# Performance work log

Hardware: AMD Instinct MI355X
Metric: run time of the kernel (lower is better)

Reference implementation:

```python
import jax, jax.numpy as jnp
import numpy as np

B, S, D, H = 2, 2048, 1024, 16
DH = D // H


def setup_inputs() -> dict:
    key = jax.random.key(0)
    ks = jax.random.split(key, 12)
    sc = 1.0 / np.sqrt(D)
    return {
        "query": jax.random.normal(ks[0], (B, S, D), jnp.float32),
        "key": jax.random.normal(ks[1], (B, S, D), jnp.float32),
        "value": jax.random.normal(ks[2], (B, S, D), jnp.float32),
        "key_mask": jax.random.randint(ks[3], (B, S), 0, 2, jnp.int32),
        "Wq": jax.random.normal(ks[4], (D, D), jnp.float32) * sc,
        "bq": jnp.zeros((D,), jnp.float32),
        "Wk": jax.random.normal(ks[5], (D, D), jnp.float32) * sc,
        "bk": jnp.zeros((D,), jnp.float32),
        "Wv": jax.random.normal(ks[6], (D, D), jnp.float32) * sc,
        "bv": jnp.zeros((D,), jnp.float32),
        "Wo": jax.random.normal(ks[7], (D, D), jnp.float32) * sc,
        "bo": jnp.zeros((D,), jnp.float32),
    }


def _shape(x):
    # (B, L, D) -> (B, H, L, DH)
    return x.reshape(B, -1, H, DH).transpose(0, 2, 1, 3)


def reference(query, key, value, key_mask, Wq, bq, Wk, bk, Wv, bv, Wo, bo):
    # linear projections (torch Linear: x @ W.T + b)
    q = _shape(query @ Wq.T + bq)  # (B,H,S,DH)
    k = _shape(key @ Wk.T + bk)
    v = _shape(value @ Wv.T + bv)

    q = q / jnp.sqrt(jnp.asarray(DH, q.dtype))
    scores = jnp.einsum("bhqd,bhkd->bhqk", q, k)  # (B,H,S,S)

    pad = (key_mask == 0)[:, None, None, :]  # (B,1,1,K)
    scores = jnp.where(pad, jnp.asarray(-1e18, scores.dtype), scores)
    attn = jax.nn.softmax(scores, axis=-1)
    attn = jnp.where(pad, jnp.asarray(0.0, attn.dtype), attn)
    # dropout p=0.0 (eval) -> identity

    ctx = jnp.einsum("bhqk,bhkd->bhqd", attn, v)
    ctx = ctx.transpose(0, 2, 1, 3).reshape(B, -1, D)  # unshape
    output = ctx @ Wo.T + bo
    return (output, attn)
```

## Files before the change

### kernel.cpp

```cpp
#include <hip/hip_runtime.h>

#define B_  2
#define S_  2048
#define D_  1024
#define H_  16
#define DH_ 64

typedef _Float16 f16;
typedef f16   f16x2 __attribute__((ext_vector_type(2)));
typedef f16   f16x4 __attribute__((ext_vector_type(4)));
typedef f16   f16x8 __attribute__((ext_vector_type(8)));
typedef float f32x4 __attribute__((ext_vector_type(4)));
typedef float f32x16 __attribute__((ext_vector_type(16)));

static __device__ __forceinline__ f16x8 ldsm8(const f16* p) {
    return *reinterpret_cast<const f16x8*>(p);
}

static __device__ __forceinline__ int swz(int row, int byteInRow) {
    return row * 128 + (byteInRow ^ ((row & 7) << 4));
}

static __device__ __forceinline__ void gll16(const void* g, void* l) {
    __builtin_amdgcn_global_load_lds(
        (const __attribute__((address_space(1))) void*)g,
        (__attribute__((address_space(3))) void*)l, 16, 0, 0);
}

static __device__ __forceinline__ unsigned pk16(float a, float b) {
    return __builtin_bit_cast(unsigned, __builtin_amdgcn_cvt_pkrtz(a, b));
}

__global__ __launch_bounds__(256)
void qkv_gemm(const float* __restrict__ Aq, const float* __restrict__ Ak,
              const float* __restrict__ Av,
              const float* __restrict__ Wq, const float* __restrict__ Wk,
              const float* __restrict__ Wv,
              const float* __restrict__ bq, const float* __restrict__ bk,
              const float* __restrict__ bv,
              f16* __restrict__ qo, f16* __restrict__ ko, f16* __restrict__ vo,
              float qscale)
{
    constexpr int K = 1024, N = 1024;
    __shared__ __align__(16) f16 As[128][40];
    __shared__ __align__(16) f16 Bs[128][40];
    const int z = blockIdx.z;
    const float* A    = z == 0 ? Aq : z == 1 ? Ak : Av;
    const float* W    = z == 0 ? Wq : z == 1 ? Wk : Wv;
    const float* bias = z == 0 ? bq : z == 1 ? bk : bv;
    const float scale = z == 0 ? qscale : 1.0f;

    const int t  = threadIdx.x;
    const int bm = blockIdx.y * 128;
    const int bn = blockIdx.x * 128;
    const int w  = t >> 6, l = t & 63;
    const int wr = w >> 1, wc = w & 1;
    const int lr = l & 15, lg = l >> 4;

    f32x4 acc[4][4];
    #pragma unroll
    for (int m = 0; m < 4; ++m)
        #pragma unroll
        for (int n = 0; n < 4; ++n)
            acc[m][n] = (f32x4){0.f, 0.f, 0.f, 0.f};

    for (int kt = 0; kt < K / 32; ++kt) {
        #pragma unroll
        for (int i = 0; i < 4; ++i) {
            int idx = t + i * 256;
            int row = idx >> 3, g = idx & 7;
            float4 v = *reinterpret_cast<const float4*>(A + (size_t)(bm + row) * K + kt * 32 + g * 4);
            alignas(8) f16 hh[4] = {(f16)v.x, (f16)v.y, (f16)v.z, (f16)v.w};
            *reinterpret_cast<uint2*>(&As[row][g * 4]) = *reinterpret_cast<uint2*>(hh);
        }
        #pragma unroll
        for (int i = 0; i < 4; ++i) {
            int idx = t + i * 256;
            int row = idx >> 3, g = idx & 7;
            float4 v = *reinterpret_cast<const float4*>(W + (size_t)(bn + row) * K + kt * 32 + g * 4);
            alignas(8) f16 hh[4] = {(f16)v.x, (f16)v.y, (f16)v.z, (f16)v.w};
            *reinterpret_cast<uint2*>(&Bs[row][g * 4]) = *reinterpret_cast<uint2*>(hh);
        }
        __syncthreads();

        f16x8 af[4], bfv[4];
        #pragma unroll
        for (int m = 0; m < 4; ++m) af[m]  = ldsm8(&As[wr * 64 + m * 16 + lr][lg * 8]);
        #pragma unroll
        for (int n = 0; n < 4; ++n) bfv[n] = ldsm8(&Bs[wc * 64 + n * 16 + lr][lg * 8]);
        #pragma unroll
        for (int m = 0; m < 4; ++m)
            #pragma unroll
            for (int n = 0; n < 4; ++n)
                acc[m][n] = __builtin_amdgcn_mfma_f32_16x16x32_f16(af[m], bfv[n], acc[m][n], 0, 0, 0);
        __syncthreads();
    }

    #pragma unroll
    for (int m = 0; m < 4; ++m) {
        #pragma unroll
        for (int n = 0; n < 4; ++n) {
            int col = bn + wc * 64 + n * 16 + lr;
            float bb = bias[col];
            if (z == 2) {
                int row0 = bm + wr * 64 + m * 16 + lg * 4;
                int b = row0 >> 11, s = row0 & 2047;
                int hh_ = col >> 6, d = col & 63;
                alignas(8) f16 hv[4];
                #pragma unroll
                for (int j = 0; j < 4; ++j)
                    hv[j] = (f16)(acc[m][n][j] + bb);
                *reinterpret_cast<uint2*>(vo +
                    (((size_t)(b * 16 + hh_) * 64 + d) * 2048 + s)) =
                    *reinterpret_cast<uint2*>(hv);
            } else {
                f16* Cp = z == 0 ? qo : ko;
                #pragma unroll
                for (int j = 0; j < 4; ++j) {
                    int row = bm + wr * 64 + m * 16 + lg * 4 + j;
                    Cp[(size_t)row * N + col] = (f16)((acc[m][n][j] + bb) * scale);
                }
            }
        }
    }
}

__global__ __launch_bounds__(256)
void gemm_out(const f16* __restrict__ A, const float* __restrict__ W,
              const float* __restrict__ bias, float* __restrict__ Cp)
{
    constexpr int K = 1024, N = 1024;
    __shared__ __align__(16) f16 As[128][40];
    __shared__ __align__(16) f16 Bs[128][40];
    const int t  = threadIdx.x;
    const int bm = blockIdx.y * 128;
    const int bn = blockIdx.x * 128;
    const int w  = t >> 6, l = t & 63;
    const int wr = w >> 1, wc = w & 1;
    const int lr = l & 15, lg = l >> 4;

    f32x4 acc[4][4];
    #pragma unroll
    for (int m = 0; m < 4; ++m)
        #pragma unroll
        for (int n = 0; n < 4; ++n)
            acc[m][n] = (f32x4){0.f, 0.f, 0.f, 0.f};

    for (int kt = 0; kt < K / 32; ++kt) {
        #pragma unroll
        for (int i = 0; i < 2; ++i) {
            int idx = t + i * 256;
            int row = idx >> 2, g = idx & 3;
            *reinterpret_cast<uint4*>(&As[row][g * 8]) =
                *reinterpret_cast<const uint4*>(A + (size_t)(bm + row) * K + kt * 32 + g * 8);
        }
        #pragma unroll
        for (int i = 0; i < 4; ++i) {
            int idx = t + i * 256;
            int row = idx >> 3, g = idx & 7;
            float4 v = *reinterpret_cast<const float4*>(W + (size_t)(bn + row) * K + kt * 32 + g * 4);
            alignas(8) f16 hh[4] = {(f16)v.x, (f16)v.y, (f16)v.z, (f16)v.w};
            *reinterpret_cast<uint2*>(&Bs[row][g * 4]) = *reinterpret_cast<uint2*>(hh);
        }
        __syncthreads();

        f16x8 af[4], bfv[4];
        #pragma unroll
        for (int m = 0; m < 4; ++m) af[m]  = ldsm8(&As[wr * 64 + m * 16 + lr][lg * 8]);
        #pragma unroll
        for (int n = 0; n < 4; ++n) bfv[n] = ldsm8(&Bs[wc * 64 + n * 16 + lr][lg * 8]);
        #pragma unroll
        for (int m = 0; m < 4; ++m)
            #pragma unroll
            for (int n = 0; n < 4; ++n)
                acc[m][n] = __builtin_amdgcn_mfma_f32_16x16x32_f16(af[m], bfv[n], acc[m][n], 0, 0, 0);
        __syncthreads();
    }

    #pragma unroll
    for (int m = 0; m < 4; ++m) {
        #pragma unroll
        for (int n = 0; n < 4; ++n) {
            int col = bn + wc * 64 + n * 16 + lr;
            float bb = bias[col];
            #pragma unroll
            for (int j = 0; j < 4; ++j) {
                int row = bm + wr * 64 + m * 16 + lg * 4 + j;
                Cp[(size_t)row * N + col] = acc[m][n][j] + bb;
            }
        }
    }
}

__global__ __launch_bounds__(512, 4)
void k_sums(const f16* __restrict__ qh, const f16* __restrict__ khp,
            const int* __restrict__ kmask, float* __restrict__ linv_g)
{
    __shared__ __align__(16) f16 ksd[2][64 * 64];
    __shared__ float red[4][32];
    __shared__ unsigned mbits[64];

    const int t  = threadIdx.x;
    const int w  = t >> 6, l = t & 63, lo = l & 31, hi = l >> 5;
    const int wq = w >> 1, wk = w & 1;

    const int bid  = blockIdx.x;
    const int xcd  = bid & 7;
    const int slot = bid >> 3;
    const int bh   = (xcd << 2) | (slot >> 4);
    const int qt   = slot & 15;
    const int b    = bh >> 4;
    const int h    = bh & 15;
    const int q0   = qt * 128;

    f16x8 qf[4];
    {
        const f16* qb = qh + (size_t)(b * S_ + q0 + wq * 32 + lo) * D_ + h * DH_ + hi * 8;
        #pragma unroll
        for (int c = 0; c < 4; ++c) qf[c] = *reinterpret_cast<const f16x8*>(qb + c * 16);
    }

    #pragma unroll
    for (int r = 0; r < 4; ++r) {
        int ktm = w * 4 + r;
        int mkv = kmask[b * S_ + ktm * 64 + l];
        unsigned long long bl = __ballot(mkv != 0);
        if (l == 0) {
            mbits[ktm * 2]     = (unsigned)bl;
            mbits[ktm * 2 + 1] = (unsigned)(bl >> 32);
        }
    }

    const int r8 = l >> 3, l8 = l & 7;
    const int xorc8 = (l8 ^ r8) * 8;
    const f16* kgb = khp + (size_t)b * S_ * D_ + h * DH_;
    const int krow = wk * 32 + lo;

    auto stageK = [&](int buf, int kt) {
        int row = w * 8 + r8;
        gll16(kgb + (size_t)(kt * 64 + row) * D_ + xorc8,
              (char*)ksd[buf] + w * 1024);
    };

    stageK(0, 0);
    __syncthreads();

    float ls = 0.f;
    int cur = 0;
    for (int kt = 0; kt < 32; ++kt) {
        if (kt + 1 < 32) stageK(cur ^ 1, kt + 1);

        const unsigned mshift = mbits[kt * 2 + wk] >> (hi * 4);

        f32x16 s;
        #pragma unroll
        for (int i = 0; i < 16; ++i) s[i] = 0.f;
        #pragma unroll
        for (int c = 0; c < 4; ++c) {
            f16x8 kf = *reinterpret_cast<const f16x8*>(
                (const char*)ksd[cur] + swz(krow, c * 32 + hi * 16));
            s = __builtin_amdgcn_mfma_f32_32x32x16_f16(kf, qf[c], s, 0, 0, 0);
        }
        #pragma unroll
        for (int q4 = 0; q4 < 4; ++q4)
            #pragma unroll
            for (int j = 0; j < 4; ++j) {
                float e = __builtin_amdgcn_exp2f(s[q4 * 4 + j]);
                ls += ((mshift >> (q4 * 8 + j)) & 1) ? e : 0.0f;
            }
        __syncthreads();
        cur ^= 1;
    }

    ls += __shfl_xor(ls, 32, 64);
    if (wk == 1 && hi == 0) red[wq][lo] = ls;
    __syncthreads();
    if (wk == 0 && hi == 0)
        linv_g[(size_t)bh * S_ + q0 + wq * 32 + lo] = 1.0f / (ls + red[wq][lo]);
}

__global__ __launch_bounds__(256, 3)
void attn_fused(const f16* __restrict__ qh, const f16* __restrict__ khp,
                const f16* __restrict__ vtg, const int* __restrict__ kmask,
                const float* __restrict__ linv_g,
                float* __restrict__ attn_out, f16* __restrict__ ch)
{
    __shared__ __align__(16) f16 ksd[2][64 * 64];
    __shared__ __align__(16) f16 vsd[2][64 * 64];
    __shared__ unsigned mbits[64];

    const int t   = threadIdx.x;
    const int w   = t >> 6, l = t & 63, lo = l & 31, hi = l >> 5;
    const int qh_ = w & 1, kh_ = w >> 1;

    const int bid  = blockIdx.x;
    const int xcd  = bid & 7;
    const int slot = bid >> 3;
    const int bh   = (xcd << 2) | (slot >> 5);
    const int qt   = slot & 31;
    const int b    = bh >> 4;
    const int h    = bh & 15;
    const int q0   = qt * 64;

    const float invl = linv_g[(size_t)bh * S_ + q0 + qh_ * 32 + lo];

    f16x8 qf[4];
    {
        const f16* qb = qh + (size_t)(b * S_ + q0 + qh_ * 32 + lo) * D_ + h * DH_ + hi * 8;
        #pragma unroll
        for (int c = 0; c < 4; ++c) qf[c] = *reinterpret_cast<const f16x8*>(qb + c * 16);
    }

    #pragma unroll
    for (int r = 0; r < 8; ++r) {
        int ktm = w * 8 + r;
        int mkv = kmask[b * S_ + ktm * 64 + l];
        unsigned long long bl = __ballot(mkv != 0);
        if (l == 0) {
            mbits[ktm * 2]     = (unsigned)bl;
            mbits[ktm * 2 + 1] = (unsigned)(bl >> 32);
        }
    }

    const int r8 = l >> 3, l8 = l & 7;
    const int xorc8 = (l8 ^ r8) * 8;
    const f16* kgb = khp + (size_t)b * S_ * D_ + h * DH_;
    const f16* vgb = vtg + (size_t)(bh * 64) * S_;
    const int krow = kh_ * 32 + lo;

    auto stageK = [&](int buf, int kt) {
        #pragma unroll
        for (int i = 0; i < 2; ++i) {
            int row = i * 32 + w * 8 + r8;
            gll16(kgb + (size_t)(kt * 64 + row) * D_ + xorc8,
                  (char*)ksd[buf] + i * 4096 + w * 1024);
        }
    };
    auto stageV = [&](int buf, int kt) {
        #pragma unroll
        for (int i = 0; i < 2; ++i) {
            int row = i * 32 + w * 8 + r8;
            gll16(vgb + (size_t)row * S_ + kt * 64 + xorc8,
                  (char*)vsd[buf] + i * 4096 + w * 1024);
        }
    };

    stageK(0, 0);
    stageV(0, 0);
    __syncthreads();

    f32x16 oc0, oc1;
    #pragma unroll
    for (int i = 0; i < 16; ++i) { oc0[i] = 0.f; oc1[i] = 0.f; }
    int cur = 0;

    float* ab = attn_out + ((size_t)((b * H_ + h) * S_ + q0 + qh_ * 32 + lo)) * S_
                + kh_ * 32 + hi * 4;

    for (int kt = 0; kt < 32; ++kt) {
        if (kt + 1 < 32) { stageK(cur ^ 1, kt + 1); stageV(cur ^ 1, kt + 1); }

        const unsigned mshift = mbits[kt * 2 + kh_] >> (hi * 4);

        f32x16 s;
        #pragma unroll
        for (int i = 0; i < 16; ++i) s[i] = 0.f;
        #pragma unroll
        for (int c = 0; c < 4; ++c) {
            f16x8 kf = *reinterpret_cast<const f16x8*>(
                (const char*)ksd[cur] + swz(krow, c * 32 + hi * 16));
            s = __builtin_amdgcn_mfma_f32_32x32x16_f16(kf, qf[c], s, 0, 0, 0);
        }

        float p[16];
        #pragma unroll
        for (int q4 = 0; q4 < 4; ++q4)
            #pragma unroll
            for (int j = 0; j < 4; ++j) {
                float e = __builtin_amdgcn_exp2f(s[q4 * 4 + j]);
                p[q4 * 4 + j] = ((mshift >> (q4 * 8 + j)) & 1) ? e : 0.0f;
            }

        #pragma unroll
        for (int q4 = 0; q4 < 4; ++q4) {
            float4 o = {p[q4 * 4 + 0] * invl, p[q4 * 4 + 1] * invl,
                        p[q4 * 4 + 2] * invl, p[q4 * 4 + 3] * invl};
            *reinterpret_cast<float4*>(ab + (size_t)kt * 64 + q4 * 8) = o;
        }

        #pragma unroll
        for (int j2 = 0; j2 < 2; ++j2) {
            unsigned wds[4], ods[4];
            #pragma unroll
            for (int i = 0; i < 4; ++i)
                wds[i] = pk16(p[8 * j2 + 2 * i], p[8 * j2 + 2 * i + 1]);
            #pragma unroll
            for (int i = 0; i < 4; ++i)
                ods[i] = (unsigned)__shfl_xor((int)wds[i], 32, 64);
            uint4 bw = (hi == 0) ? (uint4){wds[0], wds[1], ods[0], ods[1]}
                                 : (uint4){ods[2], ods[3], wds[2], wds[3]};
            f16x8 bf = __builtin_bit_cast(f16x8, bw);

            int bir = kh_ * 64 + j2 * 32 + hi * 16;
            f16x8 va0 = *reinterpret_cast<const f16x8*>((const char*)vsd[cur] + swz(lo, bir));
            f16x8 va1 = *reinterpret_cast<const f16x8*>((const char*)vsd[cur] + swz(lo + 32, bir));
            oc0 = __builtin_amdgcn_mfma_f32_32x32x16_f16(va0, bf, oc0, 0, 0, 0);
            oc1 = __builtin_amdgcn_mfma_f32_32x32x16_f16(va1, bf, oc1, 0, 0, 0);
        }
        __syncthreads();
        cur ^= 1;
    }

    float* psf = reinterpret_cast<float*>(&ksd[0][0]);
    #pragma unroll
    for (int g = 0; g < 2; ++g) {
        if (kh_ == 1 && qh_ == g) {
            #pragma unroll
            for (int r = 0; r < 16; ++r) {
                int d0 = (r & 3) + 8 * (r >> 2) + 4 * hi;
                psf[d0 * 32 + lo]        = oc0[r];
                psf[(32 + d0) * 32 + lo] = oc1[r];
            }
        }
        __syncthreads();
        if (kh_ == 0 && qh_ == g) {
            f16* cb = ch + (size_t)(b * S_ + q0 + g * 32 + lo) * D_ + h * DH_;
            #pragma unroll
            for (int q4 = 0; q4 < 4; ++q4) {
                int d0 = 8 * q4 + 4 * hi;
                f16x4 v0, v1;
                #pragma unroll
                for (int j = 0; j < 4; ++j) {
                    int r = 4 * q4 + j;
                    int dd = (r & 3) + 8 * (r >> 2) + 4 * hi;
                    v0[j] = (f16)((oc0[r] + psf[dd * 32 + lo]) * invl);
                    v1[j] = (f16)((oc1[r] + psf[(32 + dd) * 32 + lo]) * invl);
                }
                *reinterpret_cast<f16x4*>(cb + d0) = v0;
                *reinterpret_cast<f16x4*>(cb + 32 + d0) = v1;
            }
        }
        __syncthreads();
    }
}

extern "C" void kernel_launch(void* const* d_in, const int* in_sizes, int n_in,
                              void* d_out, int out_size, void* d_ws, size_t ws_size,
                              hipStream_t stream) {
    const float* query = (const float*)d_in[0];
    const float* key   = (const float*)d_in[1];
    const float* value = (const float*)d_in[2];
    const int*   kmask = (const int*)d_in[3];
    const float* Wq = (const float*)d_in[4];
    const float* bq = (const float*)d_in[5];
    const float* Wk = (const float*)d_in[6];
    const float* bk = (const float*)d_in[7];
    const float* Wv = (const float*)d_in[8];
    const float* bv = (const float*)d_in[9];
    const float* Wo = (const float*)d_in[10];
    const float* bo = (const float*)d_in[11];

    float* out  = (float*)d_out;
    float* attn = out + (size_t)B_ * S_ * D_;

    const size_t NE = (size_t)B_ * S_ * D_;
    f16* qhp = (f16*)d_ws;
    f16* khp = qhp + NE;
    f16* vtg = khp + NE;
    f16* chx = vtg + NE;
    float* linv_g = (float*)(chx + NE);

    const float qscale = 0.125f * 1.44269504088896340736f;

    qkv_gemm<<<dim3(8, 32, 3), 256, 0, stream>>>(query, key, value, Wq, Wk, Wv,
                                                 bq, bk, bv, qhp, khp, vtg, qscale);

    k_sums<<<dim3(B_ * H_ * (S_ / 128)), dim3(512), 0, stream>>>(qhp, khp, kmask, linv_g);

    attn_fused<<<dim3(B_ * H_ * (S_ / 64)), 256, 0, stream>>>(qhp, khp, vtg, kmask,
                                                              linv_g, attn, chx);

    gemm_out<<<dim3(8, 32), 256, 0, stream>>>(chx, Wo, bo, out);
}
```

Before: 337.1 us.

## Triple-buffer K/V staging with counted waits and nontemporal attention stores

The fused attention kernel moves from double to triple buffering of the K and V tiles in LDS. It now prefetches two tiles ahead and replaces the full __syncthreads with s_waitcnt vmcnt plus a raw barrier, so loads stay in flight across iterations. The large fp32 attention-probability writes now use nontemporal stores to reduce cache pollution. This costs extra LDS, which may reduce occupancy. The correctness of the hand-counted vmcnt values depends on how the global stores are counted.

```diff
diff --git a/kernel.cpp b/kernel.cpp
--- a/kernel.cpp
+++ b/kernel.cpp
@@ -285,8 +285,8 @@
                 const float* __restrict__ linv_g,
                 float* __restrict__ attn_out, f16* __restrict__ ch)
 {
-    __shared__ __align__(16) f16 ksd[2][64 * 64];
-    __shared__ __align__(16) f16 vsd[2][64 * 64];
+    __shared__ __align__(16) f16 ksd[3][64 * 64];
+    __shared__ __align__(16) f16 vsd[3][64 * 64];
     __shared__ unsigned mbits[64];
 
     const int t   = threadIdx.x;
@@ -328,26 +328,21 @@
     const f16* vgb = vtg + (size_t)(bh * 64) * S_;
     const int krow = kh_ * 32 + lo;
 
-    auto stageK = [&](int buf, int kt) {
+    auto stageKV = [&](int buf, int kt) {
         #pragma unroll
         for (int i = 0; i < 2; ++i) {
             int row = i * 32 + w * 8 + r8;
             gll16(kgb + (size_t)(kt * 64 + row) * D_ + xorc8,
-                  (char*)ksd[buf] + i * 4096 + w * 1024);
+                  (char*)ksd + buf * 8192 + i * 4096 + w * 1024);
+            gll16(vgb + (size_t)row * S_ + kt * 64 + xorc8,
+                  (char*)vsd + buf * 8192 + i * 4096 + w * 1024);
         }
     };
-    auto stageV = [&](int buf, int kt) {
-        #pragma unroll
-        for (int i = 0; i < 2; ++i) {
-            int row = i * 32 + w * 8 + r8;
-            gll16(vgb + (size_t)row * S_ + kt * 64 + xorc8,
-                  (char*)vsd[buf] + i * 4096 + w * 1024);
-        }
-    };
-
-    stageK(0, 0);
-    stageV(0, 0);
-    __syncthreads();
+
+    stageKV(0, 0);
+    stageKV(1, 1);
+    asm volatile("s_waitcnt vmcnt(4) lgkmcnt(0)" ::: "memory");
+    __builtin_amdgcn_s_barrier();
 
     f32x16 oc0, oc1;
     #pragma unroll
@@ -358,7 +353,10 @@
                 + kh_ * 32 + hi * 4;
 
     for (int kt = 0; kt < 32; ++kt) {
-        if (kt + 1 < 32) { stageK(cur ^ 1, kt + 1); stageV(cur ^ 1, kt + 1); }
+        if (kt + 2 < 32) {
+            int stg = cur + 2; if (stg >= 3) stg -= 3;
+            stageKV(stg, kt + 2);
+        }
 
         const unsigned mshift = mbits[kt * 2 + kh_] >> (hi * 4);
 
@@ -368,7 +366,7 @@
         #pragma unroll
         for (int c = 0; c < 4; ++c) {
             f16x8 kf = *reinterpret_cast<const f16x8*>(
-                (const char*)ksd[cur] + swz(krow, c * 32 + hi * 16));
+                (const char*)ksd + cur * 8192 + swz(krow, c * 32 + hi * 16));
             s = __builtin_amdgcn_mfma_f32_32x32x16_f16(kf, qf[c], s, 0, 0, 0);
         }
 
@@ -383,9 +381,10 @@
 
         #pragma unroll
         for (int q4 = 0; q4 < 4; ++q4) {
-            float4 o = {p[q4 * 4 + 0] * invl, p[q4 * 4 + 1] * invl,
-                        p[q4 * 4 + 2] * invl, p[q4 * 4 + 3] * invl};
-            *reinterpret_cast<float4*>(ab + (size_t)kt * 64 + q4 * 8) = o;
+            f32x4 o = {p[q4 * 4 + 0] * invl, p[q4 * 4 + 1] * invl,
+                       p[q4 * 4 + 2] * invl, p[q4 * 4 + 3] * invl};
+            __builtin_nontemporal_store(o,
+                reinterpret_cast<f32x4*>(ab + (size_t)kt * 64 + q4 * 8));
         }
 
         #pragma unroll
@@ -402,16 +401,21 @@
             f16x8 bf = __builtin_bit_cast(f16x8, bw);
 
             int bir = kh_ * 64 + j2 * 32 + hi * 16;
-            f16x8 va0 = *reinterpret_cast<const f16x8*>((const char*)vsd[cur] + swz(lo, bir));
-            f16x8 va1 = *reinterpret_cast<const f16x8*>((const char*)vsd[cur] + swz(lo + 32, bir));
+            f16x8 va0 = *reinterpret_cast<const f16x8*>(
+                (const char*)vsd + cur * 8192 + swz(lo, bir));
+            f16x8 va1 = *reinterpret_cast<const f16x8*>(
+                (const char*)vsd + cur * 8192 + swz(lo + 32, bir));
             oc0 = __builtin_amdgcn_mfma_f32_32x32x16_f16(va0, bf, oc0, 0, 0, 0);
             oc1 = __builtin_amdgcn_mfma_f32_32x32x16_f16(va1, bf, oc1, 0, 0, 0);
         }
-        __syncthreads();
-        cur ^= 1;
+
+        asm volatile("s_waitcnt vmcnt(8)" ::: "memory");
+        __builtin_amdgcn_s_barrier();
+        ++cur; if (cur >= 3) cur -= 3;
     }
 
     float* psf = reinterpret_cast<float*>(&ksd[0][0]);
+    __syncthreads();
     #pragma unroll
     for (int g = 0; g < 2; ++g) {
         if (kh_ == 1 && qh_ == g) {
```

Measured after the change: 753.7 us. +123.6%, slower.

## Fuse softmax row-sum pass into attention kernel with full-key-tile warps

Applied to the files above, without the earlier changes.

Removes the separate k_sums kernel and computes the softmax denominator inside attn_fused with a first pass over K, then a second pass that writes attention probabilities and accumulates P·V. Each warp now owns 32 query rows across all 64 keys of a tile, so the cross-warp LDS reduction of partial outputs at the end disappears. The grid shrinks to 128-query blocks (512 blocks of 256 threads) with 4 warps each doing 32 rows. This drops one launch and the linv round trip through global memory, but each block does more serial work, there are fewer blocks in flight, and register pressure rises.

```diff
diff --git a/kernel.cpp b/kernel.cpp
--- a/kernel.cpp
+++ b/kernel.cpp
@@ -192,17 +192,18 @@
     }
 }
 
-__global__ __launch_bounds__(512, 4)
-void k_sums(const f16* __restrict__ qh, const f16* __restrict__ khp,
-            const int* __restrict__ kmask, float* __restrict__ linv_g)
+__global__ __launch_bounds__(256, 3)
+void attn_fused(const f16* __restrict__ qh, const f16* __restrict__ khp,
+                const f16* __restrict__ vtg, const int* __restrict__ kmask,
+                float* __restrict__ attn_out, f16* __restrict__ ch)
 {
     __shared__ __align__(16) f16 ksd[2][64 * 64];
-    __shared__ float red[4][32];
+    __shared__ __align__(16) f16 vsd[2][64 * 64];
     __shared__ unsigned mbits[64];
 
     const int t  = threadIdx.x;
     const int w  = t >> 6, l = t & 63, lo = l & 31, hi = l >> 5;
-    const int wq = w >> 1, wk = w & 1;
+    const bool H1 = (hi == 1);
 
     const int bid  = blockIdx.x;
     const int xcd  = bid & 7;
@@ -212,101 +213,11 @@
     const int b    = bh >> 4;
     const int h    = bh & 15;
     const int q0   = qt * 128;
+    const int row  = q0 + w * 32 + lo;
 
     f16x8 qf[4];
     {
-        const f16* qb = qh + (size_t)(b * S_ + q0 + wq * 32 + lo) * D_ + h * DH_ + hi * 8;
-        #pragma unroll
-        for (int c = 0; c < 4; ++c) qf[c] = *reinterpret_cast<const f16x8*>(qb + c * 16);
-    }
-
-    #pragma unroll
-    for (int r = 0; r < 4; ++r) {
-        int ktm = w * 4 + r;
-        int mkv = kmask[b * S_ + ktm * 64 + l];
-        unsigned long long bl = __ballot(mkv != 0);
-        if (l == 0) {
-            mbits[ktm * 2]     = (unsigned)bl;
-            mbits[ktm * 2 + 1] = (unsigned)(bl >> 32);
-        }
-    }
-
-    const int r8 = l >> 3, l8 = l & 7;
-    const int xorc8 = (l8 ^ r8) * 8;
-    const f16* kgb = khp + (size_t)b * S_ * D_ + h * DH_;
-    const int krow = wk * 32 + lo;
-
-    auto stageK = [&](int buf, int kt) {
-        int row = w * 8 + r8;
-        gll16(kgb + (size_t)(kt * 64 + row) * D_ + xorc8,
-              (char*)ksd[buf] + w * 1024);
-    };
-
-    stageK(0, 0);
-    __syncthreads();
-
-    float ls = 0.f;
-    int cur = 0;
-    for (int kt = 0; kt < 32; ++kt) {
-        if (kt + 1 < 32) stageK(cur ^ 1, kt + 1);
-
-        const unsigned mshift = mbits[kt * 2 + wk] >> (hi * 4);
-
-        f32x16 s;
-        #pragma unroll
-        for (int i = 0; i < 16; ++i) s[i] = 0.f;
-        #pragma unroll
-        for (int c = 0; c < 4; ++c) {
-            f16x8 kf = *reinterpret_cast<const f16x8*>(
-                (const char*)ksd[cur] + swz(krow, c * 32 + hi * 16));
-            s = __builtin_amdgcn_mfma_f32_32x32x16_f16(kf, qf[c], s, 0, 0, 0);
-        }
-        #pragma unroll
-        for (int q4 = 0; q4 < 4; ++q4)
-            #pragma unroll
-            for (int j = 0; j < 4; ++j) {
-                float e = __builtin_amdgcn_exp2f(s[q4 * 4 + j]);
-                ls += ((mshift >> (q4 * 8 + j)) & 1) ? e : 0.0f;
-            }
-        __syncthreads();
-        cur ^= 1;
-    }
-
-    ls += __shfl_xor(ls, 32, 64);
-    if (wk == 1 && hi == 0) red[wq][lo] = ls;
-    __syncthreads();
-    if (wk == 0 && hi == 0)
-        linv_g[(size_t)bh * S_ + q0 + wq * 32 + lo] = 1.0f / (ls + red[wq][lo]);
-}
-
-__global__ __launch_bounds__(256, 3)
-void attn_fused(const f16* __restrict__ qh, const f16* __restrict__ khp,
-                const f16* __restrict__ vtg, const int* __restrict__ kmask,
-                const float* __restrict__ linv_g,
-                float* __restrict__ attn_out, f16* __restrict__ ch)
-{
-    __shared__ __align__(16) f16 ksd[2][64 * 64];
-    __shared__ __align__(16) f16 vsd[2][64 * 64];
-    __shared__ unsigned mbits[64];
-
-    const int t   = threadIdx.x;
-    const int w   = t >> 6, l = t & 63, lo = l & 31, hi = l >> 5;
-    const int qh_ = w & 1, kh_ = w >> 1;
-
-    const int bid  = blockIdx.x;
-    const int xcd  = bid & 7;
-    const int slot = bid >> 3;
-    const int bh   = (xcd << 2) | (slot >> 5);
-    const int qt   = slot & 31;
-    const int b    = bh >> 4;
-    const int h    = bh & 15;
-    const int q0   = qt * 64;
-
-    const float invl = linv_g[(size_t)bh * S_ + q0 + qh_ * 32 + lo];
-
-    f16x8 qf[4];
-    {
-        const f16* qb = qh + (size_t)(b * S_ + q0 + qh_ * 32 + lo) * D_ + h * DH_ + hi * 8;
+        const f16* qb = qh + (size_t)(b * S_ + row) * D_ + h * DH_ + hi * 8;
         #pragma unroll
         for (int c = 0; c < 4; ++c) qf[c] = *reinterpret_cast<const f16x8*>(qb + c * 16);
     }
@@ -326,24 +237,65 @@
     const int xorc8 = (l8 ^ r8) * 8;
     const f16* kgb = khp + (size_t)b * S_ * D_ + h * DH_;
     const f16* vgb = vtg + (size_t)(bh * 64) * S_;
-    const int krow = kh_ * 32 + lo;
 
     auto stageK = [&](int buf, int kt) {
         #pragma unroll
         for (int i = 0; i < 2; ++i) {
-            int row = i * 32 + w * 8 + r8;
-            gll16(kgb + (size_t)(kt * 64 + row) * D_ + xorc8,
-                  (char*)ksd[buf] + i * 4096 + w * 1024);
+            int rr = i * 32 + w * 8 + r8;
+            gll16(kgb + (size_t)(kt * 64 + rr) * D_ + xorc8,
+                  (char*)ksd + buf * 8192 + i * 4096 + w * 1024);
         }
     };
     auto stageV = [&](int buf, int kt) {
         #pragma unroll
         for (int i = 0; i < 2; ++i) {
-            int row = i * 32 + w * 8 + r8;
-            gll16(vgb + (size_t)row * S_ + kt * 64 + xorc8,
-                  (char*)vsd[buf] + i * 4096 + w * 1024);
+            int rr = i * 32 + w * 8 + r8;
+            gll16(vgb + (size_t)rr * S_ + kt * 64 + xorc8,
+                  (char*)vsd + buf * 8192 + i * 4096 + w * 1024);
         }
     };
+
+    stageK(0, 0);
+    __syncthreads();
+
+    float ls = 0.f;
+    int cur = 0;
+    for (int kt = 0; kt < 32; ++kt) {
+        if (kt + 1 < 32) stageK(cur ^ 1, kt + 1);
+
+        f32x16 s0, s1;
+        #pragma unroll
+        for (int i = 0; i < 16; ++i) { s0[i] = 0.f; s1[i] = 0.f; }
+        #pragma unroll
+        for (int c = 0; c < 4; ++c) {
+            f16x8 kf = *reinterpret_cast<const f16x8*>(
+                (const char*)ksd + cur * 8192 + swz(lo, c * 32 + hi * 16));
+            s0 = __builtin_amdgcn_mfma_f32_32x32x16_f16(kf, qf[c], s0, 0, 0, 0);
+        }
+        #pragma unroll
+        for (int c = 0; c < 4; ++c) {
+            f16x8 kf = *reinterpret_cast<const f16x8*>(
+                (const char*)ksd + cur * 8192 + swz(lo + 32, c * 32 + hi * 16));
+            s1 = __builtin_amdgcn_mfma_f32_32x32x16_f16(kf, qf[c], s1, 0, 0, 0);
+        }
+
+        const unsigned m0 = mbits[kt * 2]     >> (hi * 4);
+        const unsigned m1 = mbits[kt * 2 + 1] >> (hi * 4);
+        #pragma unroll
+        for (int q4 = 0; q4 < 4; ++q4)
+            #pragma unroll
+            for (int j = 0; j < 4; ++j) {
+                float e0 = __builtin_amdgcn_exp2f(s0[q4 * 4 + j]);
+                float e1 = __builtin_amdgcn_exp2f(s1[q4 * 4 + j]);
+                ls += ((m0 >> (q4 * 8 + j)) & 1) ? e0 : 0.0f;
+                ls += ((m1 >> (q4 * 8 + j)) & 1) ? e1 : 0.0f;
+            }
+        __syncthreads();
+        cur ^= 1;
+    }
+
+    ls += __shfl_xor(ls, 32, 64);
+    const float invl = 1.0f / ls;
 
     stageK(0, 0);
     stageV(0, 0);
@@ -352,95 +304,96 @@
     f32x16 oc0, oc1;
     #pragma unroll
     for (int i = 0; i < 16; ++i) { oc0[i] = 0.f; oc1[i] = 0.f; }
-    int cur = 0;
-
-    float* ab = attn_out + ((size_t)((b * H_ + h) * S_ + q0 + qh_ * 32 + lo)) * S_
-                + kh_ * 32 + hi * 4;
+    cur = 0;
+
+    float* ab = attn_out + ((size_t)bh * S_ + row) * S_ + hi * 4;
 
     for (int kt = 0; kt < 32; ++kt) {
         if (kt + 1 < 32) { stageK(cur ^ 1, kt + 1); stageV(cur ^ 1, kt + 1); }
 
-        const unsigned mshift = mbits[kt * 2 + kh_] >> (hi * 4);
-
-        f32x16 s;
-        #pragma unroll
-        for (int i = 0; i < 16; ++i) s[i] = 0.f;
+        f32x16 s0, s1;
+        #pragma unroll
+        for (int i = 0; i < 16; ++i) { s0[i] = 0.f; s1[i] = 0.f; }
         #pragma unroll
         for (int c = 0; c < 4; ++c) {
             f16x8 kf = *reinterpret_cast<const f16x8*>(
-                (const char*)ksd[cur] + swz(krow, c * 32 + hi * 16));
-            s = __builtin_amdgcn_mfma_f32_32x32x16_f16(kf, qf[c], s, 0, 0, 0);
-        }
-
-        float p[16];
+                (const char*)ksd + cur * 8192 + swz(lo, c * 32 + hi * 16));
+            s0 = __builtin_amdgcn_mfma_f32_32x32x16_f16(kf, qf[c], s0, 0, 0, 0);
+        }
+        #pragma unroll
+        for (int c = 0; c < 4; ++c) {
+            f16x8 kf = *reinterpret_cast<const f16x8*>(
+                (const char*)ksd + cur * 8192 + swz(lo + 32, c * 32 + hi * 16));
+            s1 = __builtin_amdgcn_mfma_f32_32x32x16_f16(kf, qf[c], s1, 0, 0, 0);
+        }
+
+        const unsigned m0 = mbits[kt * 2]     >> (hi * 4);
+        const unsigned m1 = mbits[kt * 2 + 1] >> (hi * 4);
+        float p0[16], p1[16];
         #pragma unroll
         for (int q4 = 0; q4 < 4; ++q4)
             #pragma unroll
             for (int j = 0; j < 4; ++j) {
-                float e = __builtin_amdgcn_exp2f(s[q4 * 4 + j]);
-                p[q4 * 4 + j] = ((mshift >> (q4 * 8 + j)) & 1) ? e : 0.0f;
+                float e0 = __builtin_amdgcn_exp2f(s0[q4 * 4 + j]);
+                float e1 = __builtin_amdgcn_exp2f(s1[q4 * 4 + j]);
+                p0[q4 * 4 + j] = ((m0 >> (q4 * 8 + j)) & 1) ? e0 : 0.0f;
+                p1[q4 * 4 + j] = ((m1 >> (q4 * 8 + j)) & 1) ? e1 : 0.0f;
             }
 
         #pragma unroll
         for (int q4 = 0; q4 < 4; ++q4) {
-            float4 o = {p[q4 * 4 + 0] * invl, p[q4 * 4 + 1] * invl,
-                        p[q4 * 4 + 2] * invl, p[q4 * 4 + 3] * invl};
-            *reinterpret_cast<float4*>(ab + (size_t)kt * 64 + q4 * 8) = o;
-        }
-
-        #pragma unroll
-        for (int j2 = 0; j2 < 2; ++j2) {
-            unsigned wds[4], ods[4];
-            #pragma unroll
-            for (int i = 0; i < 4; ++i)
-                wds[i] = pk16(p[8 * j2 + 2 * i], p[8 * j2 + 2 * i + 1]);
-            #pragma unroll
-            for (int i = 0; i < 4; ++i)
-                ods[i] = (unsigned)__shfl_xor((int)wds[i], 32, 64);
-            uint4 bw = (hi == 0) ? (uint4){wds[0], wds[1], ods[0], ods[1]}
-                                 : (uint4){ods[2], ods[3], wds[2], wds[3]};
-            f16x8 bf = __builtin_bit_cast(f16x8, bw);
-
-            int bir = kh_ * 64 + j2 * 32 + hi * 16;
-            f16x8 va0 = *reinterpret_cast<const f16x8*>((const char*)vsd[cur] + swz(lo, bir));
-            f16x8 va1 = *reinterpret_cast<const f16x8*>((const char*)vsd[cur] + swz(lo + 32, bir));
-            oc0 = __builtin_amdgcn_mfma_f32_32x32x16_f16(va0, bf, oc0, 0, 0, 0);
-            oc1 = __builtin_amdgcn_mfma_f32_32x32x16_f16(va1, bf, oc1, 0, 0, 0);
+            f32x4 o0 = {p0[q4 * 4 + 0] * invl, p0[q4 * 4 + 1] * invl,
+                        p0[q4 * 4 + 2] * invl, p0[q4 * 4 + 3] * invl};
+            *reinterpret_cast<f32x4*>(ab + (size_t)kt * 64 + q4 * 8) = o0;
+            f32x4 o1 = {p1[q4 * 4 + 0] * invl, p1[q4 * 4 + 1] * invl,
+                        p1[q4 * 4 + 2] * invl, p1[q4 * 4 + 3] * invl};
+            *reinterpret_cast<f32x4*>(ab + (size_t)kt * 64 + 32 + q4 * 8) = o1;
+        }
+
+        unsigned wa[2][4], wb[2][4];
+        #pragma unroll
+        for (int q4 = 0; q4 < 4; ++q4) {
+            wa[0][q4] = pk16(p0[q4 * 4 + 0], p0[q4 * 4 + 1]);
+            wb[0][q4] = pk16(p0[q4 * 4 + 2], p0[q4 * 4 + 3]);
+            wa[1][q4] = pk16(p1[q4 * 4 + 0], p1[q4 * 4 + 1]);
+            wb[1][q4] = pk16(p1[q4 * 4 + 2], p1[q4 * 4 + 3]);
+        }
+
+        #pragma unroll
+        for (int c2 = 0; c2 < 4; ++c2) {
+            const int hh = c2 >> 1, base = (c2 & 1) * 2;
+            unsigned a0 = wa[hh][base], a1 = wa[hh][base + 1];
+            unsigned b0 = wb[hh][base], b1 = wb[hh][base + 1];
+            unsigned sa = H1 ? a0 : a1;
+            unsigned sb = H1 ? b0 : b1;
+            unsigned ra = (unsigned)__shfl_xor((int)sa, 32, 64);
+            unsigned rb = (unsigned)__shfl_xor((int)sb, 32, 64);
+            unsigned oa = H1 ? a1 : a0;
+            unsigned ob = H1 ? b1 : b0;
+            uint4 bw = H1 ? (uint4){ra, rb, oa, ob} : (uint4){oa, ob, ra, rb};
+            f16x8 pf = __builtin_bit_cast(f16x8, bw);
+
+            f16x8 va0 = *reinterpret_cast<const f16x8*>(
+                (const char*)vsd + cur * 8192 + swz(lo, c2 * 32 + hi * 16));
+            f16x8 va1 = *reinterpret_cast<const f16x8*>(
+                (const char*)vsd + cur * 8192 + swz(lo + 32, c2 * 32 + hi * 16));
+            oc0 = __builtin_amdgcn_mfma_f32_32x32x16_f16(va0, pf, oc0, 0, 0, 0);
+            oc1 = __builtin_amdgcn_mfma_f32_32x32x16_f16(va1, pf, oc1, 0, 0, 0);
         }
         __syncthreads();
         cur ^= 1;
     }
 
-    float* psf = reinterpret_cast<float*>(&ksd[0][0]);
-    #pragma unroll
-    for (int g = 0; g < 2; ++g) {
-        if (kh_ == 1 && qh_ == g) {
-            #pragma unroll
-            for (int r = 0; r < 16; ++r) {
-                int d0 = (r & 3) + 8 * (r >> 2) + 4 * hi;
-                psf[d0 * 32 + lo]        = oc0[r];
-                psf[(32 + d0) * 32 + lo] = oc1[r];
-            }
-        }
-        __syncthreads();
-        if (kh_ == 0 && qh_ == g) {
-            f16* cb = ch + (size_t)(b * S_ + q0 + g * 32 + lo) * D_ + h * DH_;
-            #pragma unroll
-            for (int q4 = 0; q4 < 4; ++q4) {
-                int d0 = 8 * q4 + 4 * hi;
-                f16x4 v0, v1;
-                #pragma unroll
-                for (int j = 0; j < 4; ++j) {
-                    int r = 4 * q4 + j;
-                    int dd = (r & 3) + 8 * (r >> 2) + 4 * hi;
-                    v0[j] = (f16)((oc0[r] + psf[dd * 32 + lo]) * invl);
-                    v1[j] = (f16)((oc1[r] + psf[(32 + dd) * 32 + lo]) * invl);
-                }
-                *reinterpret_cast<f16x4*>(cb + d0) = v0;
-                *reinterpret_cast<f16x4*>(cb + 32 + d0) = v1;
-            }
-        }
-        __syncthreads();
+    f16* cb = ch + (size_t)(b * S_ + row) * D_ + h * DH_;
+    #pragma unroll
+    for (int q4 = 0; q4 < 4; ++q4) {
+        int d0 = 8 * q4 + 4 * hi;
+        f16x4 v0 = {(f16)(oc0[4 * q4 + 0] * invl), (f16)(oc0[4 * q4 + 1] * invl),
+                    (f16)(oc0[4 * q4 + 2] * invl), (f16)(oc0[4 * q4 + 3] * invl)};
+        *reinterpret_cast<f16x4*>(cb + d0) = v0;
+        f16x4 v1 = {(f16)(oc1[4 * q4 + 0] * invl), (f16)(oc1[4 * q4 + 1] * invl),
+                    (f16)(oc1[4 * q4 + 2] * invl), (f16)(oc1[4 * q4 + 3] * invl)};
+        *reinterpret_cast<f16x4*>(cb + 32 + d0) = v1;
     }
 }
 
@@ -468,17 +421,14 @@
     f16* khp = qhp + NE;
     f16* vtg = khp + NE;
     f16* chx = vtg + NE;
-    float* linv_g = (float*)(chx + NE);
 
     const float qscale = 0.125f * 1.44269504088896340736f;
 
     qkv_gemm<<<dim3(8, 32, 3), 256, 0, stream>>>(query, key, value, Wq, Wk, Wv,
                                                  bq, bk, bv, qhp, khp, vtg, qscale);
 
-    k_sums<<<dim3(B_ * H_ * (S_ / 128)), dim3(512), 0, stream>>>(qhp, khp, kmask, linv_g);
-
-    attn_fused<<<dim3(B_ * H_ * (S_ / 64)), 256, 0, stream>>>(qhp, khp, vtg, kmask,
-                                                              linv_g, attn, chx);
+    attn_fused<<<dim3(B_ * H_ * (S_ / 128)), 256, 0, stream>>>(qhp, khp, vtg, kmask,
+                                                               attn, chx);
 
     gemm_out<<<dim3(8, 32), 256, 0, stream>>>(chx, Wo, bo, out);
 }
```

Result: no change. 334.8 us (-0.7%).
